# Kernel tuning notes

Hardware: AMD Instinct MI355X
Metric: run time of the kernel (lower is better)

## Reference

```python
import jax, jax.numpy as jnp
import numpy as np

PATCH_SIZE = 128
NUM_PATCHES = 4


def setup_inputs() -> dict:
    key = jax.random.key(0)
    k1, k2 = jax.random.split(key)
    B, C, H, W = 32, 3, 512, 512
    images = jax.random.normal(k1, (B, C, H, W), dtype=jnp.float32)
    uncertainty_maps = jax.random.uniform(k2, (B, 1, H, W), dtype=jnp.float32)
    return {"images": images, "uncertainty_maps": uncertainty_maps}


def _select_patches(umap):
    """Greedy masked-argmax patch selection on one [H, W] uncertainty map.
    Returns coords [NUM_PATCHES, 4] int32 as (x1, y1, x2, y2)."""
    H, W = umap.shape
    eps = min(PATCH_SIZE, H // 2, W // 2)   # effective patch size (static)
    half = eps // 2
    margin = max(eps // 4, 1)
    ys = jnp.arange(H)[:, None]
    xs = jnp.arange(W)[None, :]

    def fix(a1, a2, L):
        # enforce window of exactly `eps` when clipped at the border
        small = (a2 - a1) < eps
        a2n = jnp.where(a1 == 0, jnp.minimum(L, a1 + eps), a2)
        a1n = jnp.where(a1 == 0, a1, jnp.maximum(0, a2 - eps))
        return jnp.where(small, a1n, a1), jnp.where(small, a2n, a2)

    def step(mask, _):
        masked = jnp.where(mask, -jnp.inf, umap)
        idx = jnp.argmax(masked)            # row-major first-max, same as np.ma.argmax
        yc = idx // W
        xc = idx % W
        x1 = jnp.maximum(0, xc - half)
        x2 = jnp.minimum(W, xc + half)
        y1 = jnp.maximum(0, yc - half)
        y2 = jnp.minimum(H, yc + half)
        x1, x2 = fix(x1, x2, W)
        y1, y2 = fix(y1, y2, H)
        # suppress selected region plus margin (clamping implicit in comparisons)
        box = (ys >= y1 - margin) & (ys < y2 + margin) & (xs >= x1 - margin) & (xs < x2 + margin)
        coords = jnp.stack([x1, y1, x2, y2]).astype(jnp.int32)
        return mask | box, coords

    _, coords = jax.lax.scan(step, jnp.zeros((H, W), dtype=bool), None, length=NUM_PATCHES)
    return coords  # [NUM_PATCHES, 4]


def _extract(images, coords):
    B, C, H, W = images.shape
    eps = min(PATCH_SIZE, H // 2, W // 2)

    def crop_one(img, c):
        # img [C,H,W], c = (x1,y1,x2,y2); window is always exactly eps x eps
        p = jax.lax.dynamic_slice(img, (0, c[1], c[0]), (C, eps, eps))
        if eps != PATCH_SIZE:
            # bilinear, matches F.interpolate(align_corners=False)
            p = jax.image.resize(p, (C, PATCH_SIZE, PATCH_SIZE), method="bilinear")
        return p

    return jax.vmap(jax.vmap(crop_one, in_axes=(None, 0)), in_axes=(0, 0))(images, coords)


def reference(images, uncertainty_maps):
    coords = jax.vmap(_select_patches)(uncertainty_maps[:, 0])   # [B, N, 4] int32
    patches = _extract(images, coords)                           # [B, N, C, P, P]
    return patches, coords.astype(jnp.float32)
```

## Files before the change

kernel.cpp:

```cpp
#include <hip/hip_runtime.h>
#include <math.h>
#include <float.h>

#define BN 32
#define CH 3
#define HH 512
#define WW 512
#define NP 4
#define EPS 128
#define HALF 64
#define MARGIN 32

#define NT 4096
#define PATCH_ELEMS (BN * NP * CH * EPS * EPS)
#define F4_PER_MAP (NP * CH * EPS * EPS / 4)
#define NSLICE 16
#define F4_PER_SLICE (F4_PER_MAP / NSLICE)
#define K1_NTHR 256
#define K1_NBLK (BN * NT / K1_NTHR)

__global__ __launch_bounds__(K1_NTHR)
void tile_scan(const float* __restrict__ umaps, float2* __restrict__ tiles)
{
    const int g  = blockIdx.x * K1_NTHR + threadIdx.x;
    const int b  = g >> 12;
    const int t  = g & (NT - 1);
    const int tx = t & 63, ty = t >> 6;
    const float* __restrict__ um = umaps + (size_t)b * HH * WW;
    const int x0 = tx << 3, y0 = ty << 3;
    float bv = -INFINITY; int bi = 0x7fffffff;
    #pragma unroll
    for (int r = 0; r < 8; ++r) {
        const int rowbase = (y0 + r) * WW + x0;
        const float4 a = *(const float4*)(um + rowbase);
        const float4 c = *(const float4*)(um + rowbase + 4);
        if (a.x > bv) { bv = a.x; bi = rowbase + 0; }
        if (a.y > bv) { bv = a.y; bi = rowbase + 1; }
        if (a.z > bv) { bv = a.z; bi = rowbase + 2; }
        if (a.w > bv) { bv = a.w; bi = rowbase + 3; }
        if (c.x > bv) { bv = c.x; bi = rowbase + 4; }
        if (c.y > bv) { bv = c.y; bi = rowbase + 5; }
        if (c.z > bv) { bv = c.z; bi = rowbase + 6; }
        if (c.w > bv) { bv = c.w; bi = rowbase + 7; }
    }
    tiles[g] = make_float2(bv, __int_as_float(bi));
}

__global__ __launch_bounds__(1024)
void select_extract(const float* __restrict__ images,
                    const float* __restrict__ umaps,
                    const float2* __restrict__ tiles,
                    float* __restrict__ out)
{
    const int tid   = threadIdx.x;
    const int lane  = tid & 63;
    const int wave  = tid >> 6;
    const int b     = blockIdx.x & (BN - 1);
    const int slice = blockIdx.x >> 5;
    const int nwant = slice >> 2;
    const float* __restrict__ um = umaps + (size_t)b * HH * WW;
    float* coords_out = out + PATCH_ELEMS;

    __shared__ float2   tvi[NT];
    __shared__ float2   l2[64];
    __shared__ unsigned dirty[128];
    __shared__ int      boxes[NP][4];
    __shared__ int      px1, py1;

    {
        const float4* __restrict__ src = (const float4*)(tiles + (size_t)b * NT);
        float4* dst = (float4*)tvi;
        dst[tid]        = src[tid];
        dst[tid + 1024] = src[tid + 1024];
    }
    if (tid < 128) dirty[tid] = 0u;
    if (tid < NP) { boxes[tid][0] = 0; boxes[tid][1] = 0; boxes[tid][2] = 0; boxes[tid][3] = 0; }
    __syncthreads();

    for (int r = wave; r < 64; r += 16) {
        const float2 e = tvi[(r << 6) + lane];
        float v = e.x; int ix = __float_as_int(e.y);
        #pragma unroll
        for (int off = 32; off > 0; off >>= 1) {
            const float ov = __shfl_down(v, off);
            const int   oi = __shfl_down(ix, off);
            if (ov > v || (ov == v && oi < ix)) { v = ov; ix = oi; }
        }
        if (lane == 0) l2[r] = make_float2(v, __int_as_float(ix));
    }
    __syncthreads();

    for (int k = 0; k <= nwant; ++k) {
        if (wave == 0) {
            for (;;) {
                const float2 e = l2[lane];
                float v = e.x; int ix = __float_as_int(e.y);
                #pragma unroll
                for (int off = 32; off > 0; off >>= 1) {
                    const float ov = __shfl_down(v, off);
                    const int   oi = __shfl_down(ix, off);
                    if (ov > v || (ov == v && oi < ix)) { v = ov; ix = oi; }
                }
                ix = __shfl(ix, 0);
                const int t = ((ix >> 12) << 6) | ((ix & 511) >> 3);
                const bool isdirty = (dirty[t >> 5] >> (t & 31)) & 1u;
                if (!isdirty) {
                    if (lane == 0) {
                        const int yc = ix >> 9, xc = ix & 511;
                        int x1 = max(0, xc - HALF), x2 = min(WW, xc + HALF);
                        int y1 = max(0, yc - HALF), y2 = min(HH, yc + HALF);
                        if (x2 - x1 < EPS) { if (x1 == 0) x2 = EPS; else x1 = x2 - EPS; }
                        if (y2 - y1 < EPS) { if (y1 == 0) y2 = EPS; else y1 = y2 - EPS; }
                        boxes[k][0] = max(x1 - MARGIN, 0);
                        boxes[k][1] = min(x2 + MARGIN, WW);
                        boxes[k][2] = max(y1 - MARGIN, 0);
                        boxes[k][3] = min(y2 + MARGIN, HH);
                        if (k == nwant) { px1 = x1; py1 = y1; }
                        if (slice == NSLICE - 1) {
                            const int o = (b * NP + k) * 4;
                            coords_out[o + 0] = (float)x1;
                            coords_out[o + 1] = (float)y1;
                            coords_out[o + 2] = (float)x2;
                            coords_out[o + 3] = (float)y2;
                        }
                    }
                    break;
                }
                const int ty = t >> 6, tx = t & 63;
                const int y = (ty << 3) + (lane >> 3), x = (tx << 3) + (lane & 7);
                float pv = um[y * WW + x];
                int   pi = y * WW + x;
                bool m = false;
                #pragma unroll
                for (int j = 0; j < NP; ++j)
                    m |= (y >= boxes[j][2] && y < boxes[j][3] &&
                          x >= boxes[j][0] && x < boxes[j][1]);
                if (m) { pv = -INFINITY; pi = 0x7fffffff; }
                float nv = pv; int ni = pi;
                #pragma unroll
                for (int off = 32; off > 0; off >>= 1) {
                    const float ov = __shfl_down(nv, off);
                    const int   oi = __shfl_down(ni, off);
                    if (ov > nv || (ov == nv && oi < ni)) { nv = ov; ni = oi; }
                }
                nv = __shfl(nv, 0); ni = __shfl(ni, 0);
                if (lane == 0) {
                    tvi[t] = make_float2(nv, __int_as_float(ni));
                    dirty[t >> 5] &= ~(1u << (t & 31));
                }
                const float2 e2 = tvi[(ty << 6) + lane];
                float rv; int ri;
                if (lane == tx) { rv = nv; ri = ni; }
                else            { rv = e2.x; ri = __float_as_int(e2.y); }
                #pragma unroll
                for (int off = 32; off > 0; off >>= 1) {
                    const float ov = __shfl_down(rv, off);
                    const int   oi = __shfl_down(ri, off);
                    if (ov > rv || (ov == rv && oi < ri)) { rv = ov; ri = oi; }
                }
                if (lane == 0) l2[ty] = make_float2(rv, __int_as_float(ri));
            }
        }
        __syncthreads();

        if (k == nwant) break;

        const int ex1 = boxes[k][0], ex2 = boxes[k][1];
        const int ey1 = boxes[k][2], ey2 = boxes[k][3];
        const int tx1 = ex1 >> 3, tx2 = (ex2 - 1) >> 3;
        const int ty1 = ey1 >> 3, ty2 = (ey2 - 1) >> 3;
        const int wt  = tx2 - tx1 + 1;
        const int nt2 = wt * (ty2 - ty1 + 1);
        if (tid < nt2) {
            const int tx = tx1 + tid % wt;
            const int ty = ty1 + tid / wt;
            const int t  = (ty << 6) + tx;
            const int X1 = tx << 3, Y1 = ty << 3;
            if (X1 >= ex1 && X1 + 8 <= ex2 && Y1 >= ey1 && Y1 + 8 <= ey2)
                tvi[t] = make_float2(-INFINITY, __int_as_float(0x7fffffff));
            else
                atomicOr(&dirty[t >> 5], 1u << (t & 31));
        }
        __syncthreads();

        for (int r = ty1 + wave; r <= ty2; r += 16) {
            const float2 e = tvi[(r << 6) + lane];
            float v = e.x; int ix = __float_as_int(e.y);
            #pragma unroll
            for (int off = 32; off > 0; off >>= 1) {
                const float ov = __shfl_down(v, off);
                const int   oi = __shfl_down(ix, off);
                if (ov > v || (ov == v && oi < ix)) { v = ov; ix = oi; }
            }
            if (lane == 0) l2[r] = make_float2(v, __int_as_float(ix));
        }
        __syncthreads();
    }

    const int x1 = px1, y1 = py1;
    float4* __restrict__ out4 = (float4*)out;
    #pragma unroll
    for (int it = 0; it < 3; ++it) {
        const int il  = slice * F4_PER_SLICE + (it << 10) + tid;
        const int nc  = il >> 12;
        const int c   = nc - nwant * 3;
        const int py  = (il >> 5) & 127;
        const int px0 = (il & 31) << 2;

        const float* __restrict__ src =
            images + (((size_t)b * CH + c) * HH + (y1 + py)) * WW + x1 + px0;
        out4[(size_t)b * F4_PER_MAP + il] = make_float4(src[0], src[1], src[2], src[3]);
    }
}

extern "C" void kernel_launch(void* const* d_in, const int* in_sizes, int n_in,
                              void* d_out, int out_size, void* d_ws, size_t ws_size,
                              hipStream_t stream) {
    const float* images = (const float*)d_in[0];
    const float* umaps  = (const float*)d_in[1];
    float* out          = (float*)d_out;
    float2* tiles       = (float2*)d_ws;

    tile_scan<<<K1_NBLK, K1_NTHR, 0, stream>>>(umaps, tiles);
    select_extract<<<BN * NSLICE, 1024, 0, stream>>>(images, umaps, tiles, out);
}
```

Baseline: 173.8 us.

## Fuse tile scan into extraction kernel with per-batch leader selection and flag handoff

Merges the tile-scan kernel into the main kernel. Each block scans its share of tiles, and one leader block per batch waits on an atomic counter, then runs the greedy selection once. It publishes each patch origin through a release-store flag, so the other blocks spin on their flag and copy as soon as their patch is known. This removes the redundant selection each slice block used to repeat and one kernel boundary, and halves the slice count. The cost is inter-block spin-waits that assume all blocks are co-resident, plus an extra tiny init kernel.

```diff
diff --git a/kernel.cpp b/kernel.cpp
--- a/kernel.cpp
+++ b/kernel.cpp
@@ -14,50 +14,32 @@
 #define NT 4096
 #define PATCH_ELEMS (BN * NP * CH * EPS * EPS)
 #define F4_PER_MAP (NP * CH * EPS * EPS / 4)
-#define NSLICE 16
+#define NSLICE 8
 #define F4_PER_SLICE (F4_PER_MAP / NSLICE)
-#define K1_NTHR 256
-#define K1_NBLK (BN * NT / K1_NTHR)
-
-__global__ __launch_bounds__(K1_NTHR)
-void tile_scan(const float* __restrict__ umaps, float2* __restrict__ tiles)
+#define NBLK (BN * NSLICE)
+
+
+__global__ void init_ws(int* __restrict__ done, int* __restrict__ flags)
 {
-    const int g  = blockIdx.x * K1_NTHR + threadIdx.x;
-    const int b  = g >> 12;
-    const int t  = g & (NT - 1);
-    const int tx = t & 63, ty = t >> 6;
-    const float* __restrict__ um = umaps + (size_t)b * HH * WW;
-    const int x0 = tx << 3, y0 = ty << 3;
-    float bv = -INFINITY; int bi = 0x7fffffff;
-    #pragma unroll
-    for (int r = 0; r < 8; ++r) {
-        const int rowbase = (y0 + r) * WW + x0;
-        const float4 a = *(const float4*)(um + rowbase);
-        const float4 c = *(const float4*)(um + rowbase + 4);
-        if (a.x > bv) { bv = a.x; bi = rowbase + 0; }
-        if (a.y > bv) { bv = a.y; bi = rowbase + 1; }
-        if (a.z > bv) { bv = a.z; bi = rowbase + 2; }
-        if (a.w > bv) { bv = a.w; bi = rowbase + 3; }
-        if (c.x > bv) { bv = c.x; bi = rowbase + 4; }
-        if (c.y > bv) { bv = c.y; bi = rowbase + 5; }
-        if (c.z > bv) { bv = c.z; bi = rowbase + 6; }
-        if (c.w > bv) { bv = c.w; bi = rowbase + 7; }
-    }
-    tiles[g] = make_float2(bv, __int_as_float(bi));
+    const int t = threadIdx.x;
+    if (t < BN) done[t] = 0;
+    if (t < BN * NP) flags[t] = 0;
 }
 
 __global__ __launch_bounds__(1024)
-void select_extract(const float* __restrict__ images,
-                    const float* __restrict__ umaps,
-                    const float2* __restrict__ tiles,
-                    float* __restrict__ out)
+void fused(const float* __restrict__ images,
+           const float* __restrict__ umaps,
+           float2* __restrict__ tiles,
+           int* __restrict__ done,
+           int* __restrict__ flags,
+           float* __restrict__ out)
 {
     const int tid   = threadIdx.x;
     const int lane  = tid & 63;
     const int wave  = tid >> 6;
     const int b     = blockIdx.x & (BN - 1);
     const int slice = blockIdx.x >> 5;
-    const int nwant = slice >> 2;
+    const int nwant = slice >> 1;
     const float* __restrict__ um = umaps + (size_t)b * HH * WW;
     float* coords_out = out + PATCH_ELEMS;
 
@@ -65,35 +47,164 @@
     __shared__ float2   l2[64];
     __shared__ unsigned dirty[128];
     __shared__ int      boxes[NP][4];
-    __shared__ int      px1, py1;
-
-    {
-        const float4* __restrict__ src = (const float4*)(tiles + (size_t)b * NT);
-        float4* dst = (float4*)tvi;
-        dst[tid]        = src[tid];
-        dst[tid + 1024] = src[tid + 1024];
+    __shared__ int      spx1, spy1;
+
+    if (tid < 512) {
+        const int t  = slice * 512 + tid;
+        const int tx = t & 63, ty = t >> 6;
+        const int x0 = tx << 3, y0 = ty << 3;
+        float bv = -INFINITY; int bi = 0x7fffffff;
+        #pragma unroll
+        for (int r = 0; r < 8; ++r) {
+            const int rowbase = (y0 + r) * WW + x0;
+            const float4 a = *(const float4*)(um + rowbase);
+            const float4 c = *(const float4*)(um + rowbase + 4);
+            if (a.x > bv) { bv = a.x; bi = rowbase + 0; }
+            if (a.y > bv) { bv = a.y; bi = rowbase + 1; }
+            if (a.z > bv) { bv = a.z; bi = rowbase + 2; }
+            if (a.w > bv) { bv = a.w; bi = rowbase + 3; }
+            if (c.x > bv) { bv = c.x; bi = rowbase + 4; }
+            if (c.y > bv) { bv = c.y; bi = rowbase + 5; }
+            if (c.z > bv) { bv = c.z; bi = rowbase + 6; }
+            if (c.w > bv) { bv = c.w; bi = rowbase + 7; }
+        }
+        tiles[b * NT + t] = make_float2(bv, __int_as_float(bi));
     }
-    if (tid < 128) dirty[tid] = 0u;
-    if (tid < NP) { boxes[tid][0] = 0; boxes[tid][1] = 0; boxes[tid][2] = 0; boxes[tid][3] = 0; }
+    __threadfence();
     __syncthreads();
-
-    for (int r = wave; r < 64; r += 16) {
-        const float2 e = tvi[(r << 6) + lane];
-        float v = e.x; int ix = __float_as_int(e.y);
-        #pragma unroll
-        for (int off = 32; off > 0; off >>= 1) {
-            const float ov = __shfl_down(v, off);
-            const int   oi = __shfl_down(ix, off);
-            if (ov > v || (ov == v && oi < ix)) { v = ov; ix = oi; }
-        }
-        if (lane == 0) l2[r] = make_float2(v, __int_as_float(ix));
-    }
-    __syncthreads();
-
-    for (int k = 0; k <= nwant; ++k) {
-        if (wave == 0) {
-            for (;;) {
-                const float2 e = l2[lane];
+    if (tid == 0) atomicAdd(&done[b], 1);
+
+    if (slice == 0) {
+        if (tid == 0) {
+            while (__hip_atomic_load(&done[b], __ATOMIC_ACQUIRE,
+                                     __HIP_MEMORY_SCOPE_AGENT) < NSLICE)
+                __builtin_amdgcn_s_sleep(1);
+        }
+        __syncthreads();
+        __threadfence();
+
+        {
+            const unsigned long long* __restrict__ src =
+                (const unsigned long long*)(tiles + (size_t)b * NT);
+            unsigned long long* dst = (unsigned long long*)tvi;
+            #pragma unroll
+            for (int i = 0; i < 4; ++i)
+                dst[tid + (i << 10)] = __hip_atomic_load(&src[tid + (i << 10)],
+                        __ATOMIC_RELAXED, __HIP_MEMORY_SCOPE_AGENT);
+        }
+        if (tid < 128) dirty[tid] = 0u;
+        if (tid < NP) { boxes[tid][0] = 0; boxes[tid][1] = 0; boxes[tid][2] = 0; boxes[tid][3] = 0; }
+        __syncthreads();
+
+        for (int r = wave; r < 64; r += 16) {
+            const float2 e = tvi[(r << 6) + lane];
+            float v = e.x; int ix = __float_as_int(e.y);
+            #pragma unroll
+            for (int off = 32; off > 0; off >>= 1) {
+                const float ov = __shfl_down(v, off);
+                const int   oi = __shfl_down(ix, off);
+                if (ov > v || (ov == v && oi < ix)) { v = ov; ix = oi; }
+            }
+            if (lane == 0) l2[r] = make_float2(v, __int_as_float(ix));
+        }
+        __syncthreads();
+
+        for (int k = 0; k < NP; ++k) {
+            if (wave == 0) {
+                for (;;) {
+                    const float2 e = l2[lane];
+                    float v = e.x; int ix = __float_as_int(e.y);
+                    #pragma unroll
+                    for (int off = 32; off > 0; off >>= 1) {
+                        const float ov = __shfl_down(v, off);
+                        const int   oi = __shfl_down(ix, off);
+                        if (ov > v || (ov == v && oi < ix)) { v = ov; ix = oi; }
+                    }
+                    ix = __shfl(ix, 0);
+                    const int t = ((ix >> 12) << 6) | ((ix & 511) >> 3);
+                    const bool isdirty = (dirty[t >> 5] >> (t & 31)) & 1u;
+                    if (!isdirty) {
+                        if (lane == 0) {
+                            const int yc = ix >> 9, xc = ix & 511;
+                            int x1 = max(0, xc - HALF), x2 = min(WW, xc + HALF);
+                            int y1 = max(0, yc - HALF), y2 = min(HH, yc + HALF);
+                            if (x2 - x1 < EPS) { if (x1 == 0) x2 = EPS; else x1 = x2 - EPS; }
+                            if (y2 - y1 < EPS) { if (y1 == 0) y2 = EPS; else y1 = y2 - EPS; }
+                            boxes[k][0] = max(x1 - MARGIN, 0);
+                            boxes[k][1] = min(x2 + MARGIN, WW);
+                            boxes[k][2] = max(y1 - MARGIN, 0);
+                            boxes[k][3] = min(y2 + MARGIN, HH);
+                            if (k == 0) { spx1 = x1; spy1 = y1; }
+                            const int o = (b * NP + k) * 4;
+                            coords_out[o + 0] = (float)x1;
+                            coords_out[o + 1] = (float)y1;
+                            coords_out[o + 2] = (float)x2;
+                            coords_out[o + 3] = (float)y2;
+                            __hip_atomic_store(&flags[b * NP + k],
+                                               0x40000000 | (y1 << 10) | x1,
+                                               __ATOMIC_RELEASE, __HIP_MEMORY_SCOPE_AGENT);
+                        }
+                        break;
+                    }
+                    const int ty = t >> 6, tx = t & 63;
+                    const int y = (ty << 3) + (lane >> 3), x = (tx << 3) + (lane & 7);
+                    float pv = um[y * WW + x];
+                    int   pi = y * WW + x;
+                    bool m = false;
+                    #pragma unroll
+                    for (int j = 0; j < NP; ++j)
+                        m |= (y >= boxes[j][2] && y < boxes[j][3] &&
+                              x >= boxes[j][0] && x < boxes[j][1]);
+                    if (m) { pv = -INFINITY; pi = 0x7fffffff; }
+                    float nv = pv; int ni = pi;
+                    #pragma unroll
+                    for (int off = 32; off > 0; off >>= 1) {
+                        const float ov = __shfl_down(nv, off);
+                        const int   oi = __shfl_down(ni, off);
+                        if (ov > nv || (ov == nv && oi < ni)) { nv = ov; ni = oi; }
+                    }
+                    nv = __shfl(nv, 0); ni = __shfl(ni, 0);
+                    if (lane == 0) {
+                        tvi[t] = make_float2(nv, __int_as_float(ni));
+                        dirty[t >> 5] &= ~(1u << (t & 31));
+                    }
+                    const float2 e2 = tvi[(ty << 6) + lane];
+                    float rv2; int ri2;
+                    if (lane == tx) { rv2 = nv; ri2 = ni; }
+                    else            { rv2 = e2.x; ri2 = __float_as_int(e2.y); }
+                    #pragma unroll
+                    for (int off = 32; off > 0; off >>= 1) {
+                        const float ov = __shfl_down(rv2, off);
+                        const int   oi = __shfl_down(ri2, off);
+                        if (ov > rv2 || (ov == rv2 && oi < ri2)) { rv2 = ov; ri2 = oi; }
+                    }
+                    if (lane == 0) l2[ty] = make_float2(rv2, __int_as_float(ri2));
+                }
+            }
+            __syncthreads();
+
+            if (k == NP - 1) break;
+
+            const int ex1 = boxes[k][0], ex2 = boxes[k][1];
+            const int ey1 = boxes[k][2], ey2 = boxes[k][3];
+            const int tx1 = ex1 >> 3, tx2 = (ex2 - 1) >> 3;
+            const int ty1 = ey1 >> 3, ty2 = (ey2 - 1) >> 3;
+            const int wt  = tx2 - tx1 + 1;
+            const int nt2 = wt * (ty2 - ty1 + 1);
+            if (tid < nt2) {
+                const int tx = tx1 + tid % wt;
+                const int ty = ty1 + tid / wt;
+                const int t  = (ty << 6) + tx;
+                const int X1 = tx << 3, Y1 = ty << 3;
+                if (X1 >= ex1 && X1 + 8 <= ex2 && Y1 >= ey1 && Y1 + 8 <= ey2)
+                    tvi[t] = make_float2(-INFINITY, __int_as_float(0x7fffffff));
+                else
+                    atomicOr(&dirty[t >> 5], 1u << (t & 31));
+            }
+            __syncthreads();
+
+            for (int r = ty1 + wave; r <= ty2; r += 16) {
+                const float2 e = tvi[(r << 6) + lane];
                 float v = e.x; int ix = __float_as_int(e.y);
                 #pragma unroll
                 for (int off = 32; off > 0; off >>= 1) {
@@ -101,106 +212,26 @@
                     const int   oi = __shfl_down(ix, off);
                     if (ov > v || (ov == v && oi < ix)) { v = ov; ix = oi; }
                 }
-                ix = __shfl(ix, 0);
-                const int t = ((ix >> 12) << 6) | ((ix & 511) >> 3);
-                const bool isdirty = (dirty[t >> 5] >> (t & 31)) & 1u;
-                if (!isdirty) {
-                    if (lane == 0) {
-                        const int yc = ix >> 9, xc = ix & 511;
-                        int x1 = max(0, xc - HALF), x2 = min(WW, xc + HALF);
-                        int y1 = max(0, yc - HALF), y2 = min(HH, yc + HALF);
-                        if (x2 - x1 < EPS) { if (x1 == 0) x2 = EPS; else x1 = x2 - EPS; }
-                        if (y2 - y1 < EPS) { if (y1 == 0) y2 = EPS; else y1 = y2 - EPS; }
-                        boxes[k][0] = max(x1 - MARGIN, 0);
-                        boxes[k][1] = min(x2 + MARGIN, WW);
-                        boxes[k][2] = max(y1 - MARGIN, 0);
-                        boxes[k][3] = min(y2 + MARGIN, HH);
-                        if (k == nwant) { px1 = x1; py1 = y1; }
-                        if (slice == NSLICE - 1) {
-                            const int o = (b * NP + k) * 4;
-                            coords_out[o + 0] = (float)x1;
-                            coords_out[o + 1] = (float)y1;
-                            coords_out[o + 2] = (float)x2;
-                            coords_out[o + 3] = (float)y2;
-                        }
-                    }
-                    break;
-                }
-                const int ty = t >> 6, tx = t & 63;
-                const int y = (ty << 3) + (lane >> 3), x = (tx << 3) + (lane & 7);
-                float pv = um[y * WW + x];
-                int   pi = y * WW + x;
-                bool m = false;
-                #pragma unroll
-                for (int j = 0; j < NP; ++j)
-                    m |= (y >= boxes[j][2] && y < boxes[j][3] &&
-                          x >= boxes[j][0] && x < boxes[j][1]);
-                if (m) { pv = -INFINITY; pi = 0x7fffffff; }
-                float nv = pv; int ni = pi;
-                #pragma unroll
-                for (int off = 32; off > 0; off >>= 1) {
-                    const float ov = __shfl_down(nv, off);
-                    const int   oi = __shfl_down(ni, off);
-                    if (ov > nv || (ov == nv && oi < ni)) { nv = ov; ni = oi; }
-                }
-                nv = __shfl(nv, 0); ni = __shfl(ni, 0);
-                if (lane == 0) {
-                    tvi[t] = make_float2(nv, __int_as_float(ni));
-                    dirty[t >> 5] &= ~(1u << (t & 31));
-                }
-                const float2 e2 = tvi[(ty << 6) + lane];
-                float rv; int ri;
-                if (lane == tx) { rv = nv; ri = ni; }
-                else            { rv = e2.x; ri = __float_as_int(e2.y); }
-                #pragma unroll
-                for (int off = 32; off > 0; off >>= 1) {
-                    const float ov = __shfl_down(rv, off);
-                    const int   oi = __shfl_down(ri, off);
-                    if (ov > rv || (ov == rv && oi < ri)) { rv = ov; ri = oi; }
-                }
-                if (lane == 0) l2[ty] = make_float2(rv, __int_as_float(ri));
-            }
-        }
-        __syncthreads();
-
-        if (k == nwant) break;
-
-        const int ex1 = boxes[k][0], ex2 = boxes[k][1];
-        const int ey1 = boxes[k][2], ey2 = boxes[k][3];
-        const int tx1 = ex1 >> 3, tx2 = (ex2 - 1) >> 3;
-        const int ty1 = ey1 >> 3, ty2 = (ey2 - 1) >> 3;
-        const int wt  = tx2 - tx1 + 1;
-        const int nt2 = wt * (ty2 - ty1 + 1);
-        if (tid < nt2) {
-            const int tx = tx1 + tid % wt;
-            const int ty = ty1 + tid / wt;
-            const int t  = (ty << 6) + tx;
-            const int X1 = tx << 3, Y1 = ty << 3;
-            if (X1 >= ex1 && X1 + 8 <= ex2 && Y1 >= ey1 && Y1 + 8 <= ey2)
-                tvi[t] = make_float2(-INFINITY, __int_as_float(0x7fffffff));
-            else
-                atomicOr(&dirty[t >> 5], 1u << (t & 31));
-        }
-        __syncthreads();
-
-        for (int r = ty1 + wave; r <= ty2; r += 16) {
-            const float2 e = tvi[(r << 6) + lane];
-            float v = e.x; int ix = __float_as_int(e.y);
-            #pragma unroll
-            for (int off = 32; off > 0; off >>= 1) {
-                const float ov = __shfl_down(v, off);
-                const int   oi = __shfl_down(ix, off);
-                if (ov > v || (ov == v && oi < ix)) { v = ov; ix = oi; }
-            }
-            if (lane == 0) l2[r] = make_float2(v, __int_as_float(ix));
+                if (lane == 0) l2[r] = make_float2(v, __int_as_float(ix));
+            }
+            __syncthreads();
+        }
+    } else {
+        if (tid == 0) {
+            int f;
+            while (((f = __hip_atomic_load(&flags[b * NP + nwant], __ATOMIC_ACQUIRE,
+                                           __HIP_MEMORY_SCOPE_AGENT)) >> 30) == 0)
+                __builtin_amdgcn_s_sleep(1);
+            spx1 = f & 1023;
+            spy1 = (f >> 10) & 1023;
         }
         __syncthreads();
     }
 
-    const int x1 = px1, y1 = py1;
+    const int x1 = spx1, y1 = spy1;
     float4* __restrict__ out4 = (float4*)out;
     #pragma unroll
-    for (int it = 0; it < 3; ++it) {
+    for (int it = 0; it < 6; ++it) {
         const int il  = slice * F4_PER_SLICE + (it << 10) + tid;
         const int nc  = il >> 12;
         const int c   = nc - nwant * 3;
@@ -220,7 +251,9 @@
     const float* umaps  = (const float*)d_in[1];
     float* out          = (float*)d_out;
     float2* tiles       = (float2*)d_ws;
-
-    tile_scan<<<K1_NBLK, K1_NTHR, 0, stream>>>(umaps, tiles);
-    select_extract<<<BN * NSLICE, 1024, 0, stream>>>(images, umaps, tiles, out);
+    int*    done        = (int*)((char*)d_ws + (size_t)BN * NT * sizeof(float2));
+    int*    flags       = done + BN;
+
+    init_ws<<<1, 256, 0, stream>>>(done, flags);
+    fused<<<NBLK, 1024, 0, stream>>>(images, umaps, tiles, done, flags, out);
 }
```

Measured after the change: 377.8 us. +117.4%, slower.

## Fuse tile scan and selection into one cooperative kernel with grid sync

Applied to the files above, without the earlier changes.

Merges the tile-max scan kernel into the select/extract kernel through a cooperative launch and a grid-wide sync, which removes one launch and the gap between kernels. Each block now scans 512 tiles and also writes per-row maxima to global memory, so later blocks skip the initial row reduction. Slices per image drop from 16 to 8 so the 256 blocks can be co-resident, and each block copies twice as much patch data. Blocks that extract patch 0 skip the greedy loop entirely, and output stores become nontemporal. The grid sync adds a global barrier, and fewer blocks may reduce memory-level parallelism in the copy phase.

```diff
diff --git a/kernel.cpp b/kernel.cpp
--- a/kernel.cpp
+++ b/kernel.cpp
@@ -1,6 +1,9 @@
 #include <hip/hip_runtime.h>
+#include <hip/hip_cooperative_groups.h>
 #include <math.h>
 #include <float.h>
+
+namespace cg = cooperative_groups;
 
 #define BN 32
 #define CH 3
@@ -14,50 +17,25 @@
 #define NT 4096
 #define PATCH_ELEMS (BN * NP * CH * EPS * EPS)
 #define F4_PER_MAP (NP * CH * EPS * EPS / 4)
-#define NSLICE 16
+#define NSLICE 8
 #define F4_PER_SLICE (F4_PER_MAP / NSLICE)
-#define K1_NTHR 256
-#define K1_NBLK (BN * NT / K1_NTHR)
-
-__global__ __launch_bounds__(K1_NTHR)
-void tile_scan(const float* __restrict__ umaps, float2* __restrict__ tiles)
-{
-    const int g  = blockIdx.x * K1_NTHR + threadIdx.x;
-    const int b  = g >> 12;
-    const int t  = g & (NT - 1);
-    const int tx = t & 63, ty = t >> 6;
-    const float* __restrict__ um = umaps + (size_t)b * HH * WW;
-    const int x0 = tx << 3, y0 = ty << 3;
-    float bv = -INFINITY; int bi = 0x7fffffff;
-    #pragma unroll
-    for (int r = 0; r < 8; ++r) {
-        const int rowbase = (y0 + r) * WW + x0;
-        const float4 a = *(const float4*)(um + rowbase);
-        const float4 c = *(const float4*)(um + rowbase + 4);
-        if (a.x > bv) { bv = a.x; bi = rowbase + 0; }
-        if (a.y > bv) { bv = a.y; bi = rowbase + 1; }
-        if (a.z > bv) { bv = a.z; bi = rowbase + 2; }
-        if (a.w > bv) { bv = a.w; bi = rowbase + 3; }
-        if (c.x > bv) { bv = c.x; bi = rowbase + 4; }
-        if (c.y > bv) { bv = c.y; bi = rowbase + 5; }
-        if (c.z > bv) { bv = c.z; bi = rowbase + 6; }
-        if (c.w > bv) { bv = c.w; bi = rowbase + 7; }
-    }
-    tiles[g] = make_float2(bv, __int_as_float(bi));
-}
+#define NBLK (BN * NSLICE)
+
+typedef float nf4 __attribute__((ext_vector_type(4)));
 
 __global__ __launch_bounds__(1024)
-void select_extract(const float* __restrict__ images,
-                    const float* __restrict__ umaps,
-                    const float2* __restrict__ tiles,
-                    float* __restrict__ out)
+void fused(const float* __restrict__ images,
+           const float* __restrict__ umaps,
+           float2* __restrict__ tiles,
+           float2* __restrict__ l2g,
+           float* __restrict__ out)
 {
     const int tid   = threadIdx.x;
     const int lane  = tid & 63;
     const int wave  = tid >> 6;
     const int b     = blockIdx.x & (BN - 1);
     const int slice = blockIdx.x >> 5;
-    const int nwant = slice >> 2;
+    const int nwant = slice >> 1;
     const float* __restrict__ um = umaps + (size_t)b * HH * WW;
     float* coords_out = out + PATCH_ELEMS;
 
@@ -65,35 +43,169 @@
     __shared__ float2   l2[64];
     __shared__ unsigned dirty[128];
     __shared__ int      boxes[NP][4];
-    __shared__ int      px1, py1;
-
-    {
-        const float4* __restrict__ src = (const float4*)(tiles + (size_t)b * NT);
-        float4* dst = (float4*)tvi;
-        dst[tid]        = src[tid];
-        dst[tid + 1024] = src[tid + 1024];
-    }
-    if (tid < 128) dirty[tid] = 0u;
-    if (tid < NP) { boxes[tid][0] = 0; boxes[tid][1] = 0; boxes[tid][2] = 0; boxes[tid][3] = 0; }
-    __syncthreads();
-
-    for (int r = wave; r < 64; r += 16) {
-        const float2 e = tvi[(r << 6) + lane];
-        float v = e.x; int ix = __float_as_int(e.y);
+    __shared__ int      spx1, spy1;
+
+    if (tid < 512) {
+        const int t  = slice * 512 + tid;
+        const int tx = lane;
+        const int ty = t >> 6;
+        const int x0 = tx << 3, y0 = ty << 3;
+        float bv = -INFINITY; int bi = 0x7fffffff;
+        #pragma unroll
+        for (int r = 0; r < 8; ++r) {
+            const int rowbase = (y0 + r) * WW + x0;
+            const float4 a = *(const float4*)(um + rowbase);
+            const float4 c = *(const float4*)(um + rowbase + 4);
+            if (a.x > bv) { bv = a.x; bi = rowbase + 0; }
+            if (a.y > bv) { bv = a.y; bi = rowbase + 1; }
+            if (a.z > bv) { bv = a.z; bi = rowbase + 2; }
+            if (a.w > bv) { bv = a.w; bi = rowbase + 3; }
+            if (c.x > bv) { bv = c.x; bi = rowbase + 4; }
+            if (c.y > bv) { bv = c.y; bi = rowbase + 5; }
+            if (c.z > bv) { bv = c.z; bi = rowbase + 6; }
+            if (c.w > bv) { bv = c.w; bi = rowbase + 7; }
+        }
+        tiles[b * NT + t] = make_float2(bv, __int_as_float(bi));
+        float rv = bv; int ri = bi;
         #pragma unroll
         for (int off = 32; off > 0; off >>= 1) {
-            const float ov = __shfl_down(v, off);
-            const int   oi = __shfl_down(ix, off);
-            if (ov > v || (ov == v && oi < ix)) { v = ov; ix = oi; }
-        }
-        if (lane == 0) l2[r] = make_float2(v, __int_as_float(ix));
+            const float ov = __shfl_down(rv, off);
+            const int   oi = __shfl_down(ri, off);
+            if (ov > rv || (ov == rv && oi < ri)) { rv = ov; ri = oi; }
+        }
+        if (lane == 0) l2g[b * 64 + ty] = make_float2(rv, __int_as_float(ri));
     }
-    __syncthreads();
-
-    for (int k = 0; k <= nwant; ++k) {
+    __threadfence();
+    cg::this_grid().sync();
+
+    if (nwant == 0) {
         if (wave == 0) {
-            for (;;) {
-                const float2 e = l2[lane];
+            const float2 e = l2g[b * 64 + lane];
+            float v = e.x; int ix = __float_as_int(e.y);
+            #pragma unroll
+            for (int off = 32; off > 0; off >>= 1) {
+                const float ov = __shfl_down(v, off);
+                const int   oi = __shfl_down(ix, off);
+                if (ov > v || (ov == v && oi < ix)) { v = ov; ix = oi; }
+            }
+            ix = __shfl(ix, 0);
+            if (lane == 0) {
+                const int yc = ix >> 9, xc = ix & 511;
+                int x1 = max(0, xc - HALF), x2 = min(WW, xc + HALF);
+                int y1 = max(0, yc - HALF), y2 = min(HH, yc + HALF);
+                if (x2 - x1 < EPS) { if (x1 == 0) x2 = EPS; else x1 = x2 - EPS; }
+                if (y2 - y1 < EPS) { if (y1 == 0) y2 = EPS; else y1 = y2 - EPS; }
+                spx1 = x1; spy1 = y1;
+            }
+        }
+        __syncthreads();
+    } else {
+        {
+            const float4* __restrict__ src = (const float4*)(tiles + (size_t)b * NT);
+            float4* dst = (float4*)tvi;
+            dst[tid]        = src[tid];
+            dst[tid + 1024] = src[tid + 1024];
+        }
+        if (tid < 64)  l2[tid] = l2g[b * 64 + tid];
+        if (tid < 128) dirty[tid] = 0u;
+        if (tid < NP)  { boxes[tid][0] = 0; boxes[tid][1] = 0; boxes[tid][2] = 0; boxes[tid][3] = 0; }
+        __syncthreads();
+
+        for (int k = 0; k <= nwant; ++k) {
+            if (wave == 0) {
+                for (;;) {
+                    const float2 e = l2[lane];
+                    float v = e.x; int ix = __float_as_int(e.y);
+                    #pragma unroll
+                    for (int off = 32; off > 0; off >>= 1) {
+                        const float ov = __shfl_down(v, off);
+                        const int   oi = __shfl_down(ix, off);
+                        if (ov > v || (ov == v && oi < ix)) { v = ov; ix = oi; }
+                    }
+                    ix = __shfl(ix, 0);
+                    const int t = ((ix >> 12) << 6) | ((ix & 511) >> 3);
+                    const bool isdirty = (dirty[t >> 5] >> (t & 31)) & 1u;
+                    if (!isdirty) {
+                        if (lane == 0) {
+                            const int yc = ix >> 9, xc = ix & 511;
+                            int x1 = max(0, xc - HALF), x2 = min(WW, xc + HALF);
+                            int y1 = max(0, yc - HALF), y2 = min(HH, yc + HALF);
+                            if (x2 - x1 < EPS) { if (x1 == 0) x2 = EPS; else x1 = x2 - EPS; }
+                            if (y2 - y1 < EPS) { if (y1 == 0) y2 = EPS; else y1 = y2 - EPS; }
+                            boxes[k][0] = max(x1 - MARGIN, 0);
+                            boxes[k][1] = min(x2 + MARGIN, WW);
+                            boxes[k][2] = max(y1 - MARGIN, 0);
+                            boxes[k][3] = min(y2 + MARGIN, HH);
+                            if (k == nwant) { spx1 = x1; spy1 = y1; }
+                            if (slice == NSLICE - 1) {
+                                const int o = (b * NP + k) * 4;
+                                coords_out[o + 0] = (float)x1;
+                                coords_out[o + 1] = (float)y1;
+                                coords_out[o + 2] = (float)x2;
+                                coords_out[o + 3] = (float)y2;
+                            }
+                        }
+                        break;
+                    }
+                    const int ty = t >> 6, tx = t & 63;
+                    const int y = (ty << 3) + (lane >> 3), x = (tx << 3) + (lane & 7);
+                    float pv = um[y * WW + x];
+                    int   pi = y * WW + x;
+                    bool m = false;
+                    #pragma unroll
+                    for (int j = 0; j < NP; ++j)
+                        m |= (y >= boxes[j][2] && y < boxes[j][3] &&
+                              x >= boxes[j][0] && x < boxes[j][1]);
+                    if (m) { pv = -INFINITY; pi = 0x7fffffff; }
+                    float nv = pv; int ni = pi;
+                    #pragma unroll
+                    for (int off = 32; off > 0; off >>= 1) {
+                        const float ov = __shfl_down(nv, off);
+                        const int   oi = __shfl_down(ni, off);
+                        if (ov > nv || (ov == nv && oi < ni)) { nv = ov; ni = oi; }
+                    }
+                    nv = __shfl(nv, 0); ni = __shfl(ni, 0);
+                    if (lane == 0) {
+                        tvi[t] = make_float2(nv, __int_as_float(ni));
+                        dirty[t >> 5] &= ~(1u << (t & 31));
+                    }
+                    const float2 e2 = tvi[(ty << 6) + lane];
+                    float rv2; int ri2;
+                    if (lane == tx) { rv2 = nv; ri2 = ni; }
+                    else            { rv2 = e2.x; ri2 = __float_as_int(e2.y); }
+                    #pragma unroll
+                    for (int off = 32; off > 0; off >>= 1) {
+                        const float ov = __shfl_down(rv2, off);
+                        const int   oi = __shfl_down(ri2, off);
+                        if (ov > rv2 || (ov == rv2 && oi < ri2)) { rv2 = ov; ri2 = oi; }
+                    }
+                    if (lane == 0) l2[ty] = make_float2(rv2, __int_as_float(ri2));
+                }
+            }
+            __syncthreads();
+
+            if (k == nwant) break;
+
+            const int ex1 = boxes[k][0], ex2 = boxes[k][1];
+            const int ey1 = boxes[k][2], ey2 = boxes[k][3];
+            const int tx1 = ex1 >> 3, tx2 = (ex2 - 1) >> 3;
+            const int ty1 = ey1 >> 3, ty2 = (ey2 - 1) >> 3;
+            const int wt  = tx2 - tx1 + 1;
+            const int nt2 = wt * (ty2 - ty1 + 1);
+            if (tid < nt2) {
+                const int tx = tx1 + tid % wt;
+                const int ty = ty1 + tid / wt;
+                const int t  = (ty << 6) + tx;
+                const int X1 = tx << 3, Y1 = ty << 3;
+                if (X1 >= ex1 && X1 + 8 <= ex2 && Y1 >= ey1 && Y1 + 8 <= ey2)
+                    tvi[t] = make_float2(-INFINITY, __int_as_float(0x7fffffff));
+                else
+                    atomicOr(&dirty[t >> 5], 1u << (t & 31));
+            }
+            __syncthreads();
+
+            for (int r = ty1 + wave; r <= ty2; r += 16) {
+                const float2 e = tvi[(r << 6) + lane];
                 float v = e.x; int ix = __float_as_int(e.y);
                 #pragma unroll
                 for (int off = 32; off > 0; off >>= 1) {
@@ -101,106 +213,16 @@
                     const int   oi = __shfl_down(ix, off);
                     if (ov > v || (ov == v && oi < ix)) { v = ov; ix = oi; }
                 }
-                ix = __shfl(ix, 0);
-                const int t = ((ix >> 12) << 6) | ((ix & 511) >> 3);
-                const bool isdirty = (dirty[t >> 5] >> (t & 31)) & 1u;
-                if (!isdirty) {
-                    if (lane == 0) {
-                        const int yc = ix >> 9, xc = ix & 511;
-                        int x1 = max(0, xc - HALF), x2 = min(WW, xc + HALF);
-                        int y1 = max(0, yc - HALF), y2 = min(HH, yc + HALF);
-                        if (x2 - x1 < EPS) { if (x1 == 0) x2 = EPS; else x1 = x2 - EPS; }
-                        if (y2 - y1 < EPS) { if (y1 == 0) y2 = EPS; else y1 = y2 - EPS; }
-                        boxes[k][0] = max(x1 - MARGIN, 0);
-                        boxes[k][1] = min(x2 + MARGIN, WW);
-                        boxes[k][2] = max(y1 - MARGIN, 0);
-                        boxes[k][3] = min(y2 + MARGIN, HH);
-                        if (k == nwant) { px1 = x1; py1 = y1; }
-                        if (slice == NSLICE - 1) {
-                            const int o = (b * NP + k) * 4;
-                            coords_out[o + 0] = (float)x1;
-                            coords_out[o + 1] = (float)y1;
-                            coords_out[o + 2] = (float)x2;
-                            coords_out[o + 3] = (float)y2;
-                        }
-                    }
-                    break;
-                }
-                const int ty = t >> 6, tx = t & 63;
-                const int y = (ty << 3) + (lane >> 3), x = (tx << 3) + (lane & 7);
-                float pv = um[y * WW + x];
-                int   pi = y * WW + x;
-                bool m = false;
-                #pragma unroll
-                for (int j = 0; j < NP; ++j)
-                    m |= (y >= boxes[j][2] && y < boxes[j][3] &&
-                          x >= boxes[j][0] && x < boxes[j][1]);
-                if (m) { pv = -INFINITY; pi = 0x7fffffff; }
-                float nv = pv; int ni = pi;
-                #pragma unroll
-                for (int off = 32; off > 0; off >>= 1) {
-                    const float ov = __shfl_down(nv, off);
-                    const int   oi = __shfl_down(ni, off);
-                    if (ov > nv || (ov == nv && oi < ni)) { nv = ov; ni = oi; }
-                }
-                nv = __shfl(nv, 0); ni = __shfl(ni, 0);
-                if (lane == 0) {
-                    tvi[t] = make_float2(nv, __int_as_float(ni));
-                    dirty[t >> 5] &= ~(1u << (t & 31));
-                }
-                const float2 e2 = tvi[(ty << 6) + lane];
-                float rv; int ri;
-                if (lane == tx) { rv = nv; ri = ni; }
-                else            { rv = e2.x; ri = __float_as_int(e2.y); }
-                #pragma unroll
-                for (int off = 32; off > 0; off >>= 1) {
-                    const float ov = __shfl_down(rv, off);
-                    const int   oi = __shfl_down(ri, off);
-                    if (ov > rv || (ov == rv && oi < ri)) { rv = ov; ri = oi; }
-                }
-                if (lane == 0) l2[ty] = make_float2(rv, __int_as_float(ri));
-            }
-        }
-        __syncthreads();
-
-        if (k == nwant) break;
-
-        const int ex1 = boxes[k][0], ex2 = boxes[k][1];
-        const int ey1 = boxes[k][2], ey2 = boxes[k][3];
-        const int tx1 = ex1 >> 3, tx2 = (ex2 - 1) >> 3;
-        const int ty1 = ey1 >> 3, ty2 = (ey2 - 1) >> 3;
-        const int wt  = tx2 - tx1 + 1;
-        const int nt2 = wt * (ty2 - ty1 + 1);
-        if (tid < nt2) {
-            const int tx = tx1 + tid % wt;
-            const int ty = ty1 + tid / wt;
-            const int t  = (ty << 6) + tx;
-            const int X1 = tx << 3, Y1 = ty << 3;
-            if (X1 >= ex1 && X1 + 8 <= ex2 && Y1 >= ey1 && Y1 + 8 <= ey2)
-                tvi[t] = make_float2(-INFINITY, __int_as_float(0x7fffffff));
-            else
-                atomicOr(&dirty[t >> 5], 1u << (t & 31));
-        }
-        __syncthreads();
-
-        for (int r = ty1 + wave; r <= ty2; r += 16) {
-            const float2 e = tvi[(r << 6) + lane];
-            float v = e.x; int ix = __float_as_int(e.y);
-            #pragma unroll
-            for (int off = 32; off > 0; off >>= 1) {
-                const float ov = __shfl_down(v, off);
-                const int   oi = __shfl_down(ix, off);
-                if (ov > v || (ov == v && oi < ix)) { v = ov; ix = oi; }
-            }
-            if (lane == 0) l2[r] = make_float2(v, __int_as_float(ix));
-        }
-        __syncthreads();
+                if (lane == 0) l2[r] = make_float2(v, __int_as_float(ix));
+            }
+            __syncthreads();
+        }
     }
 
-    const int x1 = px1, y1 = py1;
-    float4* __restrict__ out4 = (float4*)out;
+    const int x1 = spx1, y1 = spy1;
+    nf4* __restrict__ out4 = (nf4*)out;
     #pragma unroll
-    for (int it = 0; it < 3; ++it) {
+    for (int it = 0; it < 6; ++it) {
         const int il  = slice * F4_PER_SLICE + (it << 10) + tid;
         const int nc  = il >> 12;
         const int c   = nc - nwant * 3;
@@ -209,7 +231,8 @@
 
         const float* __restrict__ src =
             images + (((size_t)b * CH + c) * HH + (y1 + py)) * WW + x1 + px0;
-        out4[(size_t)b * F4_PER_MAP + il] = make_float4(src[0], src[1], src[2], src[3]);
+        const nf4 v = { src[0], src[1], src[2], src[3] };
+        __builtin_nontemporal_store(v, &out4[(size_t)b * F4_PER_MAP + il]);
     }
 }
 
@@ -220,7 +243,10 @@
     const float* umaps  = (const float*)d_in[1];
     float* out          = (float*)d_out;
     float2* tiles       = (float2*)d_ws;
-
-    tile_scan<<<K1_NBLK, K1_NTHR, 0, stream>>>(umaps, tiles);
-    select_extract<<<BN * NSLICE, 1024, 0, stream>>>(images, umaps, tiles, out);
+    float2* l2g         = tiles + (size_t)BN * NT;
+
+    void* args[] = { (void*)&images, (void*)&umaps, (void*)&tiles,
+                     (void*)&l2g, (void*)&out };
+    (void)hipLaunchCooperativeKernel((const void*)fused, dim3(NBLK), dim3(1024),
+                                     args, 0, stream);
 }
```

Result: slower. 326.1 us (+87.7%).
